# Performance work log

Hardware: AMD Instinct MI355X
Metric: run time of the kernel (lower is better)

## Reference

```python
import jax, jax.numpy as jnp
import numpy as np

N = 2048
IN_C, HID, LAT = 128, 128, 64
E_SPARSE = 65536


def gcn_conv(x, W, b, src, dst, w, n):
    # PyG GCNConv: h = D^-1/2 (A+I) D^-1/2 (x W) + b  (self-loops already in edge list)
    deg = jax.ops.segment_sum(w, dst, num_segments=n)
    dinv = jnp.where(deg > 0, jax.lax.rsqrt(deg), 0.0)
    norm = dinv[src] * w * dinv[dst]            # [E]
    h = x @ W                                   # [N, out]
    agg = jax.ops.segment_sum(h[src] * norm[:, None], dst, num_segments=n)
    return agg + b


def setup_inputs() -> dict:
    key = jax.random.key(0)
    ks = jax.random.split(key, 9)
    x = jax.random.normal(ks[0], (N, IN_C), jnp.float32)
    masked_y = jax.random.normal(ks[1], (N, N), jnp.float32)
    edge_index = jax.random.randint(ks[2], (2, E_SPARSE), 0, N, dtype=jnp.int32)
    s = 0.05
    W1 = jax.random.normal(ks[3], (IN_C, HID), jnp.float32) * s
    b1 = jnp.zeros((HID,), jnp.float32)
    Wmu = jax.random.normal(ks[4], (HID, LAT), jnp.float32) * s
    bmu = jnp.zeros((LAT,), jnp.float32)
    Wls = jax.random.normal(ks[5], (HID, LAT), jnp.float32) * s
    bls = jnp.zeros((LAT,), jnp.float32)
    return {"x": x, "masked_y": masked_y, "W1": W1, "b1": b1,
            "Wmu": Wmu, "bmu": bmu, "Wls": Wls, "bls": bls,
            "edge_index": edge_index}


def reference(x, masked_y, W1, b1, Wmu, bmu, Wls, bls, edge_index):
    n = x.shape[0]
    half = n // 2
    # masking leaves only the top-left [half, half] block of masked_y nonzero;
    # dense_to_sparse on that block -> all half*half (row, col) pairs (entries != 0 a.s.)
    rows = jnp.repeat(jnp.arange(half, dtype=edge_index.dtype), half)
    cols = jnp.tile(jnp.arange(half, dtype=edge_index.dtype), half)
    y_w = jax.nn.sigmoid(masked_y[:half, :half].reshape(-1))
    loop = jnp.arange(n, dtype=edge_index.dtype)
    src = jnp.concatenate([edge_index[0], rows, loop])
    dst = jnp.concatenate([edge_index[1], cols, loop])
    w = jnp.concatenate([jnp.ones((edge_index.shape[1],), x.dtype), y_w,
                         jnp.ones((n,), x.dtype)])
    hidden = jax.nn.relu(gcn_conv(x, W1, b1, src, dst, w, n))
    z_mu = gcn_conv(hidden, Wmu, bmu, src, dst, w, n)
    z_logstd = gcn_conv(hidden, Wls, bls, src, dst, w, n)
    return (z_mu, z_logstd)
```

## Files before the change

### kernel.cpp

```cpp
#include <hip/hip_runtime.h>

#define NN 2048
#define HALF 1024
#define CC 128
#define EE 65536
#define CAP 128

typedef unsigned short u16;

__device__ __forceinline__ float sigm(float v){ return 1.0f/(1.0f + __expf(-v)); }

__global__ __launch_bounds__(256) void k_prep(
    const float* __restrict__ my, const int* __restrict__ ei,
    float* __restrict__ colsum, int* __restrict__ cnt, u16* __restrict__ bucket)
{
  int b = blockIdx.x, t = threadIdx.x;
  if (b < 64) {
    int cb = b & 3, rb = b >> 2;
    int c = cb*256 + t;
    const float* p = my + (size_t)(rb*64)*NN + c;
    float s = 0.f;
    #pragma unroll 4
    for (int r=0;r<64;r++) s += sigm(p[(size_t)r*NN]);
    atomicAdd(&colsum[c], s);
  } else {
    int e = (b-64)*256 + t;
    int s = ei[e], d = ei[EE + e];
    int slot = atomicAdd(&cnt[d], 1);
    if (slot < CAP) bucket[d*CAP + slot] = (u16)s;
  }
}

__global__ __launch_bounds__(256) void k_dinv(const float* __restrict__ colsum,
                                              const int* __restrict__ cnt,
                                              float* __restrict__ dinv){
  int i = blockIdx.x*256 + threadIdx.x;
  float s = 1.0f + (float)cnt[i] + (i < HALF ? colsum[i] : 0.0f);
  dinv[i] = rsqrtf(s);
}

__device__ __forceinline__ void agg_row(
  const float* __restrict__ feat, const float* __restrict__ dinv,
  const int* __restrict__ cnt, const u16* __restrict__ bucket,
  float* __restrict__ AGG, int d, int f)
{
  float dd = dinv[d];
  float acc = dd * feat[(size_t)d*CC + f];
  int m = cnt[d]; m = m > CAP ? CAP : m;
  const u16* bk = bucket + d*CAP;
  for (int j=0;j<m;j++){
    int s = bk[j];
    acc += dinv[s] * feat[(size_t)s*CC + f];
  }
  AGG[(size_t)d*CC + f] = dd * acc;
}

__global__ __launch_bounds__(256) void k_spagg(
  const float* __restrict__ my, const float* __restrict__ x, const float* __restrict__ dinv,
  const int* __restrict__ cnt, const u16* __restrict__ bucket,
  float* __restrict__ Sp, float* __restrict__ AGG)
{
  int b = blockIdx.x, t = threadIdx.x;
  if (b < 4096) {
    int idx = b*256 + t;
    int r = idx >> 10, c = idx & 1023;
    Sp[idx] = sigm(my[(size_t)r*NN + c]) * dinv[r] * dinv[c];
  } else {
    int d = (b-4096)*2 + (t>>7);
    agg_row(x, dinv, cnt, bucket, AGG, d, t & 127);
  }
}

__global__ __launch_bounds__(256) void k_agg(
  const float* __restrict__ feat, const float* __restrict__ dinv,
  const int* __restrict__ cnt, const u16* __restrict__ bucket,
  float* __restrict__ AGG)
{
  int d = blockIdx.x*2 + (threadIdx.x>>7);
  agg_row(feat, dinv, cnt, bucket, AGG, d, threadIdx.x & 127);
}

__global__ __launch_bounds__(256) void k_gemm(
  const float* __restrict__ Sp, const float* __restrict__ F, float* __restrict__ AGG)
{
  int t = threadIdx.x;
  int f = t & 127, half = t >> 7;
  int dbase = blockIdx.x*16 + half*8;
  int r0 = blockIdx.y*256;
  float acc[8];
  #pragma unroll
  for (int j=0;j<8;j++) acc[j] = 0.f;
  #pragma unroll 4
  for (int r=r0; r<r0+256; ++r){
    float fv = F[(size_t)r*CC + f];
    const float4* sp4 = (const float4*)(Sp + (size_t)r*HALF + dbase);
    float4 s0 = sp4[0], s1 = sp4[1];
    acc[0] = fmaf(s0.x, fv, acc[0]);
    acc[1] = fmaf(s0.y, fv, acc[1]);
    acc[2] = fmaf(s0.z, fv, acc[2]);
    acc[3] = fmaf(s0.w, fv, acc[3]);
    acc[4] = fmaf(s1.x, fv, acc[4]);
    acc[5] = fmaf(s1.y, fv, acc[5]);
    acc[6] = fmaf(s1.z, fv, acc[6]);
    acc[7] = fmaf(s1.w, fv, acc[7]);
  }
  #pragma unroll
  for (int j=0;j<8;j++)
    atomicAdd(&AGG[(size_t)(dbase+j)*CC + f], acc[j]);
}

__global__ __launch_bounds__(256) void k_hidden(
  const float* __restrict__ AGG, const float* __restrict__ W1, const float* __restrict__ b1,
  float* __restrict__ hid)
{
  __shared__ float la[2][CC];
  int t = threadIdx.x;
  int rloc = t >> 7, k = t & 127;
  int row = blockIdx.x*2 + rloc;
  la[rloc][k] = AGG[(size_t)row*CC + k];
  __syncthreads();
  int f = k;
  float acc = b1[f];
  const float* ar = la[rloc];
  #pragma unroll 8
  for (int kk=0;kk<CC;kk++) acc = fmaf(ar[kk], W1[kk*CC + f], acc);
  hid[(size_t)row*CC + f] = acc > 0.f ? acc : 0.f;
}

__global__ __launch_bounds__(256) void k_z(
  const float* __restrict__ AGG, const float* __restrict__ Wmu, const float* __restrict__ bmu,
  const float* __restrict__ Wls, const float* __restrict__ bls,
  float* __restrict__ out)
{
  __shared__ float la[2][CC];
  int t = threadIdx.x;
  int rloc = t >> 7, k = t & 127;
  int row = blockIdx.x*2 + rloc;
  la[rloc][k] = AGG[(size_t)row*CC + k];
  __syncthreads();
  int f = k;
  const float* ar = la[rloc];
  if (f < 64) {
    float acc = bmu[f];
    #pragma unroll 8
    for (int kk=0;kk<CC;kk++) acc = fmaf(ar[kk], Wmu[kk*64 + f], acc);
    out[(size_t)row*64 + f] = acc;
  } else {
    int g = f - 64;
    float acc = bls[g];
    #pragma unroll 8
    for (int kk=0;kk<CC;kk++) acc = fmaf(ar[kk], Wls[kk*64 + g], acc);
    out[(size_t)NN*64 + (size_t)row*64 + g] = acc;
  }
}

extern "C" void kernel_launch(void* const* d_in, const int* in_sizes, int n_in,
                              void* d_out, int out_size, void* d_ws, size_t ws_size,
                              hipStream_t stream)
{
  (void)in_sizes; (void)n_in; (void)out_size; (void)ws_size;
  const float* x   = (const float*)d_in[0];
  const float* my  = (const float*)d_in[1];
  const float* W1  = (const float*)d_in[2];
  const float* b1  = (const float*)d_in[3];
  const float* Wmu = (const float*)d_in[4];
  const float* bmu = (const float*)d_in[5];
  const float* Wls = (const float*)d_in[6];
  const float* bls = (const float*)d_in[7];
  const int*   ei  = (const int*)d_in[8];
  float* out = (float*)d_out;
  char* ws = (char*)d_ws;

  float* colsum = (float*)(ws + 0);
  int*   cnt    = (int*)  (ws + 4096);
  float* dinv   = (float*)(ws + 12288);
  u16*   bucket = (u16*)  (ws + 20480);
  float* Sp     = (float*)(ws + 544768);
  float* AGG    = (float*)(ws + 4739072);
  float* hid    = (float*)(ws + 5787648);

  hipMemsetAsync(ws, 0, 12288, stream);
  k_prep<<<320, 256, 0, stream>>>(my, ei, colsum, cnt, bucket);
  k_dinv<<<8, 256, 0, stream>>>(colsum, cnt, dinv);
  k_spagg<<<5120, 256, 0, stream>>>(my, x, dinv, cnt, bucket, Sp, AGG);
  k_gemm<<<dim3(64, 4), 256, 0, stream>>>(Sp, x, AGG);
  k_hidden<<<1024, 256, 0, stream>>>(AGG, W1, b1, hid);
  k_agg<<<1024, 256, 0, stream>>>(hid, dinv, cnt, bucket, AGG);
  k_gemm<<<dim3(64, 4), 256, 0, stream>>>(Sp, hid, AGG);
  k_z<<<1024, 256, 0, stream>>>(AGG, Wmu, bmu, Wls, bls, out);
}
```

Before: 188.9 us.

## Fuse dense sigmoid block into aggregation kernel and drop materialized Sp matrix

Removes the precomputed normalized dense matrix Sp and the separate GEMM kernels. A single layer kernel now recomputes sigmoid(masked_y)·dinv on the fly while accumulating the dense half-block product with atomic adds, alongside the sparse bucket aggregation. This cuts the 4MB Sp write and reread and two launches per layer. In exchange it recomputes the sigmoid in both layers, uses a larger memset for two AGG buffers, and has only 128 blocks doing the dense part, with strided column reads of masked_y.

```diff
diff --git a/kernel.cpp b/kernel.cpp
--- a/kernel.cpp
+++ b/kernel.cpp
@@ -5,6 +5,8 @@
 #define CC 128
 #define EE 65536
 #define CAP 128
+#define RSPLIT 4
+#define RCH (HALF/RSPLIT)
 
 typedef unsigned short u16;
 
@@ -39,74 +41,59 @@
   dinv[i] = rsqrtf(s);
 }
 
-__device__ __forceinline__ void agg_row(
-  const float* __restrict__ feat, const float* __restrict__ dinv,
-  const int* __restrict__ cnt, const u16* __restrict__ bucket,
-  float* __restrict__ AGG, int d, int f)
-{
-  float dd = dinv[d];
-  float acc = dd * feat[(size_t)d*CC + f];
-  int m = cnt[d]; m = m > CAP ? CAP : m;
-  const u16* bk = bucket + d*CAP;
-  for (int j=0;j<m;j++){
-    int s = bk[j];
-    acc += dinv[s] * feat[(size_t)s*CC + f];
-  }
-  AGG[(size_t)d*CC + f] = dd * acc;
-}
-
-__global__ __launch_bounds__(256) void k_spagg(
-  const float* __restrict__ my, const float* __restrict__ x, const float* __restrict__ dinv,
-  const int* __restrict__ cnt, const u16* __restrict__ bucket,
-  float* __restrict__ Sp, float* __restrict__ AGG)
+__global__ __launch_bounds__(256) void k_layer(
+  const float* __restrict__ my, const float* __restrict__ feat, const float* __restrict__ dinv,
+  const int* __restrict__ cnt, const u16* __restrict__ bucket, float* __restrict__ AGG)
 {
   int b = blockIdx.x, t = threadIdx.x;
-  if (b < 4096) {
-    int idx = b*256 + t;
-    int r = idx >> 10, c = idx & 1023;
-    Sp[idx] = sigm(my[(size_t)r*NN + c]) * dinv[r] * dinv[c];
+  if (b < 128) {
+    int dtile = b >> 2;
+    int rc = b & 3;
+    int d = dtile*32 + (t & 31);
+    int f0 = (t >> 5) * 16;
+    float acc[16];
+    #pragma unroll
+    for (int j=0;j<16;j++) acc[j] = 0.f;
+    int r0 = rc*RCH;
+    #pragma unroll 2
+    for (int r=r0; r<r0+RCH; ++r){
+      float sv = sigm(my[(size_t)r*NN + d]) * dinv[r];
+      const float4* fp = (const float4*)(feat + (size_t)r*CC + f0);
+      float4 v0 = fp[0], v1 = fp[1], v2 = fp[2], v3 = fp[3];
+      acc[0]  = fmaf(sv, v0.x, acc[0]);
+      acc[1]  = fmaf(sv, v0.y, acc[1]);
+      acc[2]  = fmaf(sv, v0.z, acc[2]);
+      acc[3]  = fmaf(sv, v0.w, acc[3]);
+      acc[4]  = fmaf(sv, v1.x, acc[4]);
+      acc[5]  = fmaf(sv, v1.y, acc[5]);
+      acc[6]  = fmaf(sv, v1.z, acc[6]);
+      acc[7]  = fmaf(sv, v1.w, acc[7]);
+      acc[8]  = fmaf(sv, v2.x, acc[8]);
+      acc[9]  = fmaf(sv, v2.y, acc[9]);
+      acc[10] = fmaf(sv, v2.z, acc[10]);
+      acc[11] = fmaf(sv, v2.w, acc[11]);
+      acc[12] = fmaf(sv, v3.x, acc[12]);
+      acc[13] = fmaf(sv, v3.y, acc[13]);
+      acc[14] = fmaf(sv, v3.z, acc[14]);
+      acc[15] = fmaf(sv, v3.w, acc[15]);
+    }
+    float dd = dinv[d];
+    #pragma unroll
+    for (int j=0;j<16;j++)
+      atomicAdd(&AGG[(size_t)d*CC + f0 + j], acc[j]*dd);
   } else {
-    int d = (b-4096)*2 + (t>>7);
-    agg_row(x, dinv, cnt, bucket, AGG, d, t & 127);
+    int idx = b - 128;
+    int d = idx*2 + (t>>7), f = t & 127;
+    float dd = dinv[d];
+    float acc = dd * feat[(size_t)d*CC + f];
+    int m = cnt[d]; m = m > CAP ? CAP : m;
+    const u16* bk = bucket + d*CAP;
+    for (int j=0;j<m;j++){
+      int s = bk[j];
+      acc = fmaf(dinv[s], feat[(size_t)s*CC + f], acc);
+    }
+    atomicAdd(&AGG[(size_t)d*CC + f], dd*acc);
   }
-}
-
-__global__ __launch_bounds__(256) void k_agg(
-  const float* __restrict__ feat, const float* __restrict__ dinv,
-  const int* __restrict__ cnt, const u16* __restrict__ bucket,
-  float* __restrict__ AGG)
-{
-  int d = blockIdx.x*2 + (threadIdx.x>>7);
-  agg_row(feat, dinv, cnt, bucket, AGG, d, threadIdx.x & 127);
-}
-
-__global__ __launch_bounds__(256) void k_gemm(
-  const float* __restrict__ Sp, const float* __restrict__ F, float* __restrict__ AGG)
-{
-  int t = threadIdx.x;
-  int f = t & 127, half = t >> 7;
-  int dbase = blockIdx.x*16 + half*8;
-  int r0 = blockIdx.y*256;
-  float acc[8];
-  #pragma unroll
-  for (int j=0;j<8;j++) acc[j] = 0.f;
-  #pragma unroll 4
-  for (int r=r0; r<r0+256; ++r){
-    float fv = F[(size_t)r*CC + f];
-    const float4* sp4 = (const float4*)(Sp + (size_t)r*HALF + dbase);
-    float4 s0 = sp4[0], s1 = sp4[1];
-    acc[0] = fmaf(s0.x, fv, acc[0]);
-    acc[1] = fmaf(s0.y, fv, acc[1]);
-    acc[2] = fmaf(s0.z, fv, acc[2]);
-    acc[3] = fmaf(s0.w, fv, acc[3]);
-    acc[4] = fmaf(s1.x, fv, acc[4]);
-    acc[5] = fmaf(s1.y, fv, acc[5]);
-    acc[6] = fmaf(s1.z, fv, acc[6]);
-    acc[7] = fmaf(s1.w, fv, acc[7]);
-  }
-  #pragma unroll
-  for (int j=0;j<8;j++)
-    atomicAdd(&AGG[(size_t)(dbase+j)*CC + f], acc[j]);
 }
 
 __global__ __launch_bounds__(256) void k_hidden(
@@ -173,19 +160,17 @@
 
   float* colsum = (float*)(ws + 0);
   int*   cnt    = (int*)  (ws + 4096);
-  float* dinv   = (float*)(ws + 12288);
-  u16*   bucket = (u16*)  (ws + 20480);
-  float* Sp     = (float*)(ws + 544768);
-  float* AGG    = (float*)(ws + 4739072);
-  float* hid    = (float*)(ws + 5787648);
+  float* AGG1   = (float*)(ws + 12288);
+  float* AGG2   = (float*)(ws + 1060864);
+  float* dinv   = (float*)(ws + 2109440);
+  u16*   bucket = (u16*)  (ws + 2117632);
+  float* hid    = (float*)(ws + 2641920);
 
-  hipMemsetAsync(ws, 0, 12288, stream);
-  k_prep<<<320, 256, 0, stream>>>(my, ei, colsum, cnt, bucket);
-  k_dinv<<<8, 256, 0, stream>>>(colsum, cnt, dinv);
-  k_spagg<<<5120, 256, 0, stream>>>(my, x, dinv, cnt, bucket, Sp, AGG);
-  k_gemm<<<dim3(64, 4), 256, 0, stream>>>(Sp, x, AGG);
-  k_hidden<<<1024, 256, 0, stream>>>(AGG, W1, b1, hid);
-  k_agg<<<1024, 256, 0, stream>>>(hid, dinv, cnt, bucket, AGG);
-  k_gemm<<<dim3(64, 4), 256, 0, stream>>>(Sp, hid, AGG);
-  k_z<<<1024, 256, 0, stream>>>(AGG, Wmu, bmu, Wls, bls, out);
+  hipMemsetAsync(ws, 0, 2109440, stream);
+  k_prep <<<320,  256, 0, stream>>>(my, ei, colsum, cnt, bucket);
+  k_dinv <<<8,    256, 0, stream>>>(colsum, cnt, dinv);
+  k_layer<<<1152, 256, 0, stream>>>(my, x,   dinv, cnt, bucket, AGG1);
+  k_hidden<<<1024,256, 0, stream>>>(AGG1, W1, b1, hid);
+  k_layer<<<1152, 256, 0, stream>>>(my, hid, dinv, cnt, bucket, AGG2);
+  k_z    <<<1024, 256, 0, stream>>>(AGG2, Wmu, bmu, Wls, bls, out);
 }
```

New measurement: 270.8 us. +43.4%, slower.

## Store raw sigmoid block in prep, fuse dense GEMM with sparse aggregation per layer

Applied to the files above, without the earlier changes.

The sigmoid of the masked block is now computed once in the prep kernel, with float4 loads, and stored unscaled. The dinv normalisation moves into the GEMM, applied to the feature rows and the output rows. The separate Sp-building pass and the second read of masked_y go away, and the dense GEMM and sparse edge aggregation run as one launch that accumulates atomically into zeroed buffers, so two launches are dropped. The small W1/Wmu/Wls matmul kernels now process 8 rows per block with 4 accumulators per thread to reuse weight loads. The trade-off is a larger memset and extra atomics on the sparse path.

```diff
diff --git a/kernel.cpp b/kernel.cpp
--- a/kernel.cpp
+++ b/kernel.cpp
@@ -12,19 +12,27 @@
 
 __global__ __launch_bounds__(256) void k_prep(
     const float* __restrict__ my, const int* __restrict__ ei,
-    float* __restrict__ colsum, int* __restrict__ cnt, u16* __restrict__ bucket)
+    float* __restrict__ SpRaw, float* __restrict__ colsum,
+    int* __restrict__ cnt, u16* __restrict__ bucket)
 {
   int b = blockIdx.x, t = threadIdx.x;
-  if (b < 64) {
-    int cb = b & 3, rb = b >> 2;
-    int c = cb*256 + t;
-    const float* p = my + (size_t)(rb*64)*NN + c;
-    float s = 0.f;
-    #pragma unroll 4
-    for (int r=0;r<64;r++) s += sigm(p[(size_t)r*NN]);
-    atomicAdd(&colsum[c], s);
+  if (b < 128) {
+    int c0 = t*4;
+    float cs0=0.f, cs1=0.f, cs2=0.f, cs3=0.f;
+    #pragma unroll 2
+    for (int rr=0; rr<8; ++rr){
+      int r = b*8 + rr;
+      float4 v = *(const float4*)(my + (size_t)r*NN + c0);
+      float s0=sigm(v.x), s1=sigm(v.y), s2=sigm(v.z), s3=sigm(v.w);
+      *(float4*)(SpRaw + (size_t)r*HALF + c0) = make_float4(s0,s1,s2,s3);
+      cs0+=s0; cs1+=s1; cs2+=s2; cs3+=s3;
+    }
+    atomicAdd(&colsum[c0+0], cs0);
+    atomicAdd(&colsum[c0+1], cs1);
+    atomicAdd(&colsum[c0+2], cs2);
+    atomicAdd(&colsum[c0+3], cs3);
   } else {
-    int e = (b-64)*256 + t;
+    int e = (b-128)*256 + t;
     int s = ei[e], d = ei[EE + e];
     int slot = atomicAdd(&cnt[d], 1);
     if (slot < CAP) bucket[d*CAP + slot] = (u16)s;
@@ -39,92 +47,79 @@
   dinv[i] = rsqrtf(s);
 }
 
-__device__ __forceinline__ void agg_row(
-  const float* __restrict__ feat, const float* __restrict__ dinv,
-  const int* __restrict__ cnt, const u16* __restrict__ bucket,
-  float* __restrict__ AGG, int d, int f)
-{
-  float dd = dinv[d];
-  float acc = dd * feat[(size_t)d*CC + f];
-  int m = cnt[d]; m = m > CAP ? CAP : m;
-  const u16* bk = bucket + d*CAP;
-  for (int j=0;j<m;j++){
-    int s = bk[j];
-    acc += dinv[s] * feat[(size_t)s*CC + f];
-  }
-  AGG[(size_t)d*CC + f] = dd * acc;
-}
-
-__global__ __launch_bounds__(256) void k_spagg(
-  const float* __restrict__ my, const float* __restrict__ x, const float* __restrict__ dinv,
-  const int* __restrict__ cnt, const u16* __restrict__ bucket,
-  float* __restrict__ Sp, float* __restrict__ AGG)
+__global__ __launch_bounds__(256) void k_layer(
+  const float* __restrict__ SpRaw, const float* __restrict__ F, const float* __restrict__ dinv,
+  const int* __restrict__ cnt, const u16* __restrict__ bucket, float* __restrict__ AGG)
 {
   int b = blockIdx.x, t = threadIdx.x;
-  if (b < 4096) {
-    int idx = b*256 + t;
-    int r = idx >> 10, c = idx & 1023;
-    Sp[idx] = sigm(my[(size_t)r*NN + c]) * dinv[r] * dinv[c];
+  if (b < 256) {
+    int f = t & 127, half = t >> 7;
+    int dbase = (b>>2)*16 + half*8;
+    int r0 = (b&3)*256;
+    float acc[8];
+    #pragma unroll
+    for (int j=0;j<8;j++) acc[j] = 0.f;
+    #pragma unroll 4
+    for (int r=r0; r<r0+256; ++r){
+      float fv = F[(size_t)r*CC + f] * dinv[r];
+      const float4* sp4 = (const float4*)(SpRaw + (size_t)r*HALF + dbase);
+      float4 s0 = sp4[0], s1 = sp4[1];
+      acc[0] = fmaf(s0.x, fv, acc[0]);
+      acc[1] = fmaf(s0.y, fv, acc[1]);
+      acc[2] = fmaf(s0.z, fv, acc[2]);
+      acc[3] = fmaf(s0.w, fv, acc[3]);
+      acc[4] = fmaf(s1.x, fv, acc[4]);
+      acc[5] = fmaf(s1.y, fv, acc[5]);
+      acc[6] = fmaf(s1.z, fv, acc[6]);
+      acc[7] = fmaf(s1.w, fv, acc[7]);
+    }
+    #pragma unroll
+    for (int j=0;j<8;j++)
+      atomicAdd(&AGG[(size_t)(dbase+j)*CC + f], acc[j]*dinv[dbase+j]);
   } else {
-    int d = (b-4096)*2 + (t>>7);
-    agg_row(x, dinv, cnt, bucket, AGG, d, t & 127);
+    int idx = b - 256;
+    int d = idx*2 + (t>>7), f = t & 127;
+    float dd = dinv[d];
+    float acc = dd * F[(size_t)d*CC + f];
+    int m = cnt[d]; m = m > CAP ? CAP : m;
+    const u16* bk = bucket + d*CAP;
+    for (int j=0;j<m;j++){
+      int s = bk[j];
+      acc = fmaf(dinv[s], F[(size_t)s*CC + f], acc);
+    }
+    atomicAdd(&AGG[(size_t)d*CC + f], dd*acc);
   }
-}
-
-__global__ __launch_bounds__(256) void k_agg(
-  const float* __restrict__ feat, const float* __restrict__ dinv,
-  const int* __restrict__ cnt, const u16* __restrict__ bucket,
-  float* __restrict__ AGG)
-{
-  int d = blockIdx.x*2 + (threadIdx.x>>7);
-  agg_row(feat, dinv, cnt, bucket, AGG, d, threadIdx.x & 127);
-}
-
-__global__ __launch_bounds__(256) void k_gemm(
-  const float* __restrict__ Sp, const float* __restrict__ F, float* __restrict__ AGG)
-{
-  int t = threadIdx.x;
-  int f = t & 127, half = t >> 7;
-  int dbase = blockIdx.x*16 + half*8;
-  int r0 = blockIdx.y*256;
-  float acc[8];
-  #pragma unroll
-  for (int j=0;j<8;j++) acc[j] = 0.f;
-  #pragma unroll 4
-  for (int r=r0; r<r0+256; ++r){
-    float fv = F[(size_t)r*CC + f];
-    const float4* sp4 = (const float4*)(Sp + (size_t)r*HALF + dbase);
-    float4 s0 = sp4[0], s1 = sp4[1];
-    acc[0] = fmaf(s0.x, fv, acc[0]);
-    acc[1] = fmaf(s0.y, fv, acc[1]);
-    acc[2] = fmaf(s0.z, fv, acc[2]);
-    acc[3] = fmaf(s0.w, fv, acc[3]);
-    acc[4] = fmaf(s1.x, fv, acc[4]);
-    acc[5] = fmaf(s1.y, fv, acc[5]);
-    acc[6] = fmaf(s1.z, fv, acc[6]);
-    acc[7] = fmaf(s1.w, fv, acc[7]);
-  }
-  #pragma unroll
-  for (int j=0;j<8;j++)
-    atomicAdd(&AGG[(size_t)(dbase+j)*CC + f], acc[j]);
 }
 
 __global__ __launch_bounds__(256) void k_hidden(
   const float* __restrict__ AGG, const float* __restrict__ W1, const float* __restrict__ b1,
   float* __restrict__ hid)
 {
-  __shared__ float la[2][CC];
+  __shared__ float la[8][CC];
   int t = threadIdx.x;
-  int rloc = t >> 7, k = t & 127;
-  int row = blockIdx.x*2 + rloc;
-  la[rloc][k] = AGG[(size_t)row*CC + k];
+  int row0 = blockIdx.x*8;
+  #pragma unroll
+  for (int i=0;i<4;i++){
+    int idx = i*256 + t;
+    la[idx>>7][idx&127] = AGG[(size_t)row0*CC + idx];
+  }
   __syncthreads();
-  int f = k;
-  float acc = b1[f];
-  const float* ar = la[rloc];
-  #pragma unroll 8
-  for (int kk=0;kk<CC;kk++) acc = fmaf(ar[kk], W1[kk*CC + f], acc);
-  hid[(size_t)row*CC + f] = acc > 0.f ? acc : 0.f;
+  int f = t & 127, rh = t >> 7;
+  float acc[4];
+  float bb = b1[f];
+  #pragma unroll
+  for (int i=0;i<4;i++) acc[i] = bb;
+  #pragma unroll 4
+  for (int kk=0;kk<CC;kk++){
+    float w = W1[kk*CC + f];
+    #pragma unroll
+    for (int i=0;i<4;i++) acc[i] = fmaf(la[rh*4+i][kk], w, acc[i]);
+  }
+  #pragma unroll
+  for (int i=0;i<4;i++){
+    float v = acc[i];
+    hid[(size_t)(row0 + rh*4 + i)*CC + f] = v > 0.f ? v : 0.f;
+  }
 }
 
 __global__ __launch_bounds__(256) void k_z(
@@ -132,26 +127,32 @@
   const float* __restrict__ Wls, const float* __restrict__ bls,
   float* __restrict__ out)
 {
-  __shared__ float la[2][CC];
+  __shared__ float la[8][CC];
   int t = threadIdx.x;
-  int rloc = t >> 7, k = t & 127;
-  int row = blockIdx.x*2 + rloc;
-  la[rloc][k] = AGG[(size_t)row*CC + k];
+  int row0 = blockIdx.x*8;
+  #pragma unroll
+  for (int i=0;i<4;i++){
+    int idx = i*256 + t;
+    la[idx>>7][idx&127] = AGG[(size_t)row0*CC + idx];
+  }
   __syncthreads();
-  int f = k;
-  const float* ar = la[rloc];
-  if (f < 64) {
-    float acc = bmu[f];
-    #pragma unroll 8
-    for (int kk=0;kk<CC;kk++) acc = fmaf(ar[kk], Wmu[kk*64 + f], acc);
-    out[(size_t)row*64 + f] = acc;
-  } else {
-    int g = f - 64;
-    float acc = bls[g];
-    #pragma unroll 8
-    for (int kk=0;kk<CC;kk++) acc = fmaf(ar[kk], Wls[kk*64 + g], acc);
-    out[(size_t)NN*64 + (size_t)row*64 + g] = acc;
+  int f = t & 127, rh = t >> 7;
+  const float* W = (f < 64) ? Wmu : Wls;
+  int g = f & 63;
+  float bb = (f < 64) ? bmu[g] : bls[g];
+  size_t obase = (f < 64) ? 0 : (size_t)NN*64;
+  float acc[4];
+  #pragma unroll
+  for (int i=0;i<4;i++) acc[i] = bb;
+  #pragma unroll 4
+  for (int kk=0;kk<CC;kk++){
+    float w = W[kk*64 + g];
+    #pragma unroll
+    for (int i=0;i<4;i++) acc[i] = fmaf(la[rh*4+i][kk], w, acc[i]);
   }
+  #pragma unroll
+  for (int i=0;i<4;i++)
+    out[obase + (size_t)(row0 + rh*4 + i)*64 + g] = acc[i];
 }
 
 extern "C" void kernel_launch(void* const* d_in, const int* in_sizes, int n_in,
@@ -173,19 +174,18 @@
 
   float* colsum = (float*)(ws + 0);
   int*   cnt    = (int*)  (ws + 4096);
-  float* dinv   = (float*)(ws + 12288);
-  u16*   bucket = (u16*)  (ws + 20480);
-  float* Sp     = (float*)(ws + 544768);
-  float* AGG    = (float*)(ws + 4739072);
-  float* hid    = (float*)(ws + 5787648);
+  float* AGG1   = (float*)(ws + 12288);
+  float* AGG2   = (float*)(ws + 1060864);
+  float* dinv   = (float*)(ws + 2109440);
+  u16*   bucket = (u16*)  (ws + 2117632);
+  float* SpRaw  = (float*)(ws + 2641920);
+  float* hid    = (float*)(ws + 6836224);
 
-  hipMemsetAsync(ws, 0, 12288, stream);
-  k_prep<<<320, 256, 0, stream>>>(my, ei, colsum, cnt, bucket);
-  k_dinv<<<8, 256, 0, stream>>>(colsum, cnt, dinv);
-  k_spagg<<<5120, 256, 0, stream>>>(my, x, dinv, cnt, bucket, Sp, AGG);
-  k_gemm<<<dim3(64, 4), 256, 0, stream>>>(Sp, x, AGG);
-  k_hidden<<<1024, 256, 0, stream>>>(AGG, W1, b1, hid);
-  k_agg<<<1024, 256, 0, stream>>>(hid, dinv, cnt, bucket, AGG);
-  k_gemm<<<dim3(64, 4), 256, 0, stream>>>(Sp, hid, AGG);
-  k_z<<<1024, 256, 0, stream>>>(AGG, Wmu, bmu, Wls, bls, out);
+  hipMemsetAsync(ws, 0, 2109440, stream);
+  k_prep  <<<384,  256, 0, stream>>>(my, ei, SpRaw, colsum, cnt, bucket);
+  k_dinv  <<<8,    256, 0, stream>>>(colsum, cnt, dinv);
+  k_layer <<<1280, 256, 0, stream>>>(SpRaw, x,   dinv, cnt, bucket, AGG1);
+  k_hidden<<<256,  256, 0, stream>>>(AGG1, W1, b1, hid);
+  k_layer <<<1280, 256, 0, stream>>>(SpRaw, hid, dinv, cnt, bucket, AGG2);
+  k_z     <<<256,  256, 0, stream>>>(AGG2, Wmu, bmu, Wls, bls, out);
 }
```

Measured after the change: 178.9 us. 5.3% less time.
